# Performance work log

Measured on AMD Instinct MI355X. Metric: run time of the kernel, lower is better.

The kernel has to match this reference:

```python
import jax, jax.numpy as jnp
import numpy as np
import math

B, LQ, LK, D, H = 4, 1024, 1024, 1024, 16
DK = D // H
SCALE = 1.0 / math.sqrt(DK)
NEG_INF = -1.0e9


def setup_inputs() -> dict:
    key = jax.random.key(0)
    ks = jax.random.split(key, 18)
    w = lambda k: (jax.random.normal(k, (D, D), dtype=jnp.float32) * 0.02)
    b = lambda k: (jax.random.normal(k, (D,), dtype=jnp.float32) * 0.02)
    mask = jax.random.randint(ks[4], (B, 1, LK), 0, 2).astype(jnp.int32)
    mask = mask.at[..., 0].set(1)  # ensure at least one valid key per row
    return {
        "query": jax.random.normal(ks[0], (B, LQ, D), dtype=jnp.float32),
        "key": jax.random.normal(ks[1], (B, LK, D), dtype=jnp.float32),
        "value": jax.random.normal(ks[2], (B, LK, D), dtype=jnp.float32),
        "weak_rela": jax.random.normal(ks[3], (B, LK, D), dtype=jnp.float32),
        "mask": mask,
        "Wq": w(ks[5]), "bq": b(ks[6]),
        "Wk": w(ks[7]), "bk": b(ks[8]),
        "Wv": w(ks[9]), "bv": b(ks[10]),
        "Wrk": w(ks[11]), "brk": b(ks[12]),
        "Wrv": w(ks[13]), "brv": b(ks[14]),
        "Wo": w(ks[15]), "bo": b(ks[16]),
    }


def _proj(x, W, bias):
    # x: [B, L, D] -> [B, H, L, DK]; torch Linear: y = x @ W.T + b
    y = x @ W.T + bias
    Bn, L, _ = y.shape
    return y.reshape(Bn, L, H, DK).transpose(0, 2, 1, 3)


def reference(query, key, value, weak_rela, mask,
              Wq, bq, Wk, bk, Wv, bv, Wrk, brk, Wrv, brv, Wo, bo):
    q = _proj(query, Wq, bq)        # [B,H,LQ,DK]
    k = _proj(key, Wk, bk)          # [B,H,LK,DK]
    v = _proj(value, Wv, bv)        # [B,H,LK,DK]
    rk = _proj(weak_rela, Wrk, brk) # [B,H,LK,DK]
    rv = _proj(weak_rela, Wrv, brv) # [B,H,LK,DK]

    qk = jnp.einsum('bhqd,bhkd->bhqk', q, k) * SCALE
    qr = jnp.einsum('bhqd,bhkd->bhqk', q, rk) * SCALE

    m = (mask[:, None, :, :] == 0)  # [B,1,1,LK] broadcast over heads/queries
    qk = jnp.where(m, NEG_INF, qk)
    qr = jnp.where(m, NEG_INF, qr)

    p_vis = jax.nn.softmax(qk, axis=-1)
    p_rel = jax.nn.softmax(qr, axis=-1)

    x = (jnp.einsum('bhqk,bhkd->bhqd', p_vis, v)
         + jnp.einsum('bhqk,bhkd->bhqd', p_rel, rv))  # [B,H,LQ,DK]
    x = x.transpose(0, 2, 1, 3).reshape(query.shape[0], -1, H * DK)
    return x @ Wo.T + bo
```

## Files before the change

### kernel.cpp

```cpp
#include <hip/hip_runtime.h>
#include <stdint.h>

#define NB 4
#define NH 16
#define DKH 64
#define DMODEL 1024
#define SEQ 1024
#define SCALE 0.125f
#define NEG_INF -1.0e9f
#define K2E 0.18033688011112042f

typedef __bf16 bf16_t;
typedef __bf16 bf16x8 __attribute__((ext_vector_type(8)));
typedef __bf16 bf16x4v __attribute__((ext_vector_type(4)));
typedef float f32x4 __attribute__((ext_vector_type(4)));

typedef const uint32_t __attribute__((address_space(1)))* gas_ptr;
typedef uint32_t __attribute__((address_space(3)))* las_ptr;

__device__ __forceinline__ void gload_lds16(const void* g, void* l) {
  __builtin_amdgcn_global_load_lds((gas_ptr)g, (las_ptr)l, 16, 0, 0);
}


__global__ void cvt_multi(const float* __restrict__ i0, const float* __restrict__ i1,
                          const float* __restrict__ i2, const float* __restrict__ i3,
                          const float* __restrict__ i4, const float* __restrict__ i5,
                          bf16_t* o0, bf16_t* o1, bf16_t* o2, bf16_t* o3, bf16_t* o4, bf16_t* o5,
                          int n) {
  const int t = blockIdx.y;
  const float* in = (t == 0) ? i0 : (t == 1) ? i1 : (t == 2) ? i2 : (t == 3) ? i3 : (t == 4) ? i4 : i5;
  bf16_t* out = (t == 0) ? o0 : (t == 1) ? o1 : (t == 2) ? o2 : (t == 3) ? o3 : (t == 4) ? o4 : o5;
  const int idx = (blockIdx.x * 256 + threadIdx.x) * 4;
  if (idx >= n) return;
  const float4 v = *(const float4*)(in + idx);
  bf16x4v p;
  p[0] = (bf16_t)v.x; p[1] = (bf16_t)v.y; p[2] = (bf16_t)v.z; p[3] = (bf16_t)v.w;
  *(bf16x4v*)(out + idx) = p;
}

#define NXE ((size_t)NB * SEQ * DMODEL)
#define NWE ((size_t)DMODEL * DMODEL)
__global__ void __launch_bounds__(256, 2)
proj_gemm(const bf16_t* __restrict__ Xbase, const bf16_t* __restrict__ Wbase,
          bf16_t* __restrict__ Obase,
          const float* __restrict__ b0, const float* __restrict__ b1,
          const float* __restrict__ b2, const float* __restrict__ b3,
          const float* __restrict__ b4) {
  __shared__ bf16_t As[128 * 64];
  __shared__ bf16_t Bs[64 * 64];
  const int tid = threadIdx.x;
  const int lane = tid & 63;
  const int w = tid >> 6;
  const int wm = w >> 1, wn = w & 1;
  const int g = lane >> 4, c = lane & 15;
  const int bid = blockIdx.x;
  const int lid = (bid & 7) * 320 + (bid >> 3);
  const int seg = lid >> 9;
  const int rr = lid & 511;
  const int bm = rr >> 4, bn = rr & 15;
  const int m0 = bm * 128, n0 = bn * 64;
  const int lrow = lane >> 3;
  const int lcol = ((lane & 7) * 8) ^ ((lane >> 3) << 3);
  const int sc = (c & 7) << 3;

  const bf16_t* A = Xbase + (size_t)((seg < 3) ? seg : 3) * NXE;
  const bf16_t* W = Wbase + (size_t)seg * NWE;
  const int ooff = (seg == 0) ? 0 : (seg == 1) ? 1 : (seg == 2) ? 3 : (seg == 3) ? 2 : 4;
  bf16_t* out = Obase + (size_t)ooff * NXE;
  const float* bias = (seg == 0) ? b0 : (seg == 1) ? b1 : (seg == 2) ? b2 : (seg == 3) ? b3 : b4;
  const bool tr = (seg == 2) || (seg == 4);

  f32x4 acc[4][2] = {};

  for (int kt = 0; kt < DMODEL; kt += 64) {
#pragma unroll
    for (int p = 0; p < 4; ++p) {
      const int row = w * 32 + p * 8;
      gload_lds16(A + (size_t)(m0 + row + lrow) * DMODEL + kt + lcol, &As[row * 64]);
    }
#pragma unroll
    for (int p = 0; p < 2; ++p) {
      const int row = w * 16 + p * 8;
      gload_lds16(W + (size_t)(n0 + row + lrow) * DMODEL + kt + lcol, &Bs[row * 64]);
    }
    __syncthreads();
    bf16x8 af[4][2], bfr[2][2];
#pragma unroll
    for (int i = 0; i < 4; ++i)
#pragma unroll
      for (int kk = 0; kk < 2; ++kk)
        af[i][kk] = *(const bf16x8*)&As[(wm * 64 + i * 16 + c) * 64 + ((kk * 32 + g * 8) ^ sc)];
#pragma unroll
    for (int j = 0; j < 2; ++j)
#pragma unroll
      for (int kk = 0; kk < 2; ++kk)
        bfr[j][kk] = *(const bf16x8*)&Bs[(wn * 32 + j * 16 + c) * 64 + ((kk * 32 + g * 8) ^ sc)];
#pragma unroll
    for (int i = 0; i < 4; ++i)
#pragma unroll
      for (int j = 0; j < 2; ++j) {
        acc[i][j] = __builtin_amdgcn_mfma_f32_16x16x32_bf16(af[i][0], bfr[j][0], acc[i][j], 0, 0, 0);
        acc[i][j] = __builtin_amdgcn_mfma_f32_16x16x32_bf16(af[i][1], bfr[j][1], acc[i][j], 0, 0, 0);
      }
    __syncthreads();
  }

  float bv2[2];
#pragma unroll
  for (int j = 0; j < 2; ++j) bv2[j] = bias[n0 + wn * 32 + j * 16 + c];

#pragma unroll
  for (int i = 0; i < 4; ++i) {
    const int mrow = m0 + wm * 64 + i * 16 + g * 4;
    const int b_ = mrow >> 10, l_ = mrow & 1023;
#pragma unroll
    for (int j = 0; j < 2; ++j) {
      const int n = n0 + wn * 32 + j * 16 + c;
      const int h_ = n >> 6, dk_ = n & 63;
      if (!tr) {
#pragma unroll
        for (int r = 0; r < 4; ++r)
          out[((size_t)(b_ * NH + h_) * SEQ + l_ + r) * DKH + dk_] =
              (bf16_t)(acc[i][j][r] + bv2[j]);
      } else {
        bf16x4v pk;
#pragma unroll
        for (int r = 0; r < 4; ++r) pk[r] = (bf16_t)(acc[i][j][r] + bv2[j]);
        *(bf16x4v*)&out[((size_t)(b_ * NH + h_) * DKH + dk_) * SEQ + l_] = pk;
      }
    }
  }
}

__global__ void __launch_bounds__(256, 2)
out_gemm(const bf16_t* __restrict__ A, const bf16_t* __restrict__ W,
         const float* __restrict__ bias, float* __restrict__ out) {
  __shared__ bf16_t As[128 * 64];
  __shared__ bf16_t Bs[64 * 64];
  const int tid = threadIdx.x;
  const int lane = tid & 63;
  const int w = tid >> 6;
  const int wm = w >> 1, wn = w & 1;
  const int g = lane >> 4, c = lane & 15;
  const int bid = blockIdx.x;
  const int lid = (bid & 7) * 64 + (bid >> 3);
  const int bm = lid >> 4, bn = lid & 15;
  const int m0 = bm * 128, n0 = bn * 64;
  const int lrow = lane >> 3;
  const int lcol = ((lane & 7) * 8) ^ ((lane >> 3) << 3);
  const int sc = (c & 7) << 3;

  f32x4 acc[4][2] = {};

  for (int kt = 0; kt < DMODEL; kt += 64) {
#pragma unroll
    for (int p = 0; p < 4; ++p) {
      const int row = w * 32 + p * 8;
      gload_lds16(A + (size_t)(m0 + row + lrow) * DMODEL + kt + lcol, &As[row * 64]);
    }
#pragma unroll
    for (int p = 0; p < 2; ++p) {
      const int row = w * 16 + p * 8;
      gload_lds16(W + (size_t)(n0 + row + lrow) * DMODEL + kt + lcol, &Bs[row * 64]);
    }
    __syncthreads();
    bf16x8 af[4][2], bfr[2][2];
#pragma unroll
    for (int i = 0; i < 4; ++i)
#pragma unroll
      for (int kk = 0; kk < 2; ++kk)
        af[i][kk] = *(const bf16x8*)&As[(wm * 64 + i * 16 + c) * 64 + ((kk * 32 + g * 8) ^ sc)];
#pragma unroll
    for (int j = 0; j < 2; ++j)
#pragma unroll
      for (int kk = 0; kk < 2; ++kk)
        bfr[j][kk] = *(const bf16x8*)&Bs[(wn * 32 + j * 16 + c) * 64 + ((kk * 32 + g * 8) ^ sc)];
#pragma unroll
    for (int i = 0; i < 4; ++i)
#pragma unroll
      for (int j = 0; j < 2; ++j) {
        acc[i][j] = __builtin_amdgcn_mfma_f32_16x16x32_bf16(af[i][0], bfr[j][0], acc[i][j], 0, 0, 0);
        acc[i][j] = __builtin_amdgcn_mfma_f32_16x16x32_bf16(af[i][1], bfr[j][1], acc[i][j], 0, 0, 0);
      }
    __syncthreads();
  }

  float bv2[2];
#pragma unroll
  for (int j = 0; j < 2; ++j) bv2[j] = bias[n0 + wn * 32 + j * 16 + c];
#pragma unroll
  for (int i = 0; i < 4; ++i) {
    const int mrow = m0 + wm * 64 + i * 16 + g * 4;
#pragma unroll
    for (int j = 0; j < 2; ++j) {
      const int n = n0 + wn * 32 + j * 16 + c;
#pragma unroll
      for (int r = 0; r < 4; ++r)
        out[(size_t)(mrow + r) * DMODEL + n] = acc[i][j][r] + bv2[j];
    }
  }
}

__device__ __forceinline__ void attn_step(
    const bf16_t* __restrict__ Kt, const bf16_t* __restrict__ Vt,
    bf16_t* __restrict__ Pw, const bf16x8 (&qf)[2], const int4 (&mk)[4],
    float& m_s, float& l_s, f32x4 (&o_s)[4], int lane) {
  const int g = lane >> 4, c = lane & 15;
  const int sc = (c & 7) << 3;

  f32x4 s[4];
#pragma unroll
  for (int f = 0; f < 4; ++f) {
    const bf16x8 k0 = *(const bf16x8*)&Kt[(f * 16 + c) * 64 + ((g * 8) ^ sc)];
    const bf16x8 k1 = *(const bf16x8*)&Kt[(f * 16 + c) * 64 + ((32 + g * 8) ^ sc)];
    f32x4 a = {0.f, 0.f, 0.f, 0.f};
    a = __builtin_amdgcn_mfma_f32_16x16x32_bf16(k0, qf[0], a, 0, 0, 0);
    a = __builtin_amdgcn_mfma_f32_16x16x32_bf16(k1, qf[1], a, 0, 0, 0);
    s[f] = a;
  }

#pragma unroll
  for (int f = 0; f < 4; ++f) {
    s[f][0] = (mk[f].x == 0) ? NEG_INF : s[f][0] * K2E;
    s[f][1] = (mk[f].y == 0) ? NEG_INF : s[f][1] * K2E;
    s[f][2] = (mk[f].z == 0) ? NEG_INF : s[f][2] * K2E;
    s[f][3] = (mk[f].w == 0) ? NEG_INF : s[f][3] * K2E;
  }

  float tm = fmaxf(fmaxf(s[0][0], s[0][1]), fmaxf(s[0][2], s[0][3]));
#pragma unroll
  for (int f = 1; f < 4; ++f)
    tm = fmaxf(tm, fmaxf(fmaxf(s[f][0], s[f][1]), fmaxf(s[f][2], s[f][3])));
  tm = fmaxf(tm, __shfl_xor(tm, 16));
  tm = fmaxf(tm, __shfl_xor(tm, 32));

  const float mnew = fmaxf(m_s, tm);
  const float sf = __builtin_amdgcn_exp2f(m_s - mnew);
  m_s = mnew;

  float pf[4];
#pragma unroll
  for (int f = 0; f < 4; ++f) {
#pragma unroll
    for (int r = 0; r < 4; ++r) s[f][r] = __builtin_amdgcn_exp2f(s[f][r] - mnew);
    pf[f] = (s[f][0] + s[f][1]) + (s[f][2] + s[f][3]);
  }
  l_s = l_s * sf + ((pf[0] + pf[1]) + (pf[2] + pf[3]));
#pragma unroll
  for (int jd = 0; jd < 4; ++jd)
#pragma unroll
    for (int r = 0; r < 4; ++r) o_s[jd][r] *= sf;

#pragma unroll
  for (int f = 0; f < 4; ++f) {
    bf16x4v pk;
#pragma unroll
    for (int r = 0; r < 4; ++r) pk[r] = (bf16_t)s[f][r];
    *(bf16x4v*)&Pw[c * 64 + ((f * 16 + g * 4) ^ sc)] = pk;
  }

  const bf16x8 pa0 = *(const bf16x8*)&Pw[c * 64 + ((g * 8) ^ sc)];
  const bf16x8 pa1 = *(const bf16x8*)&Pw[c * 64 + ((32 + g * 8) ^ sc)];
#pragma unroll
  for (int jd = 0; jd < 4; ++jd) {
    const bf16x8 v0 = *(const bf16x8*)&Vt[(jd * 16 + c) * 64 + ((g * 8) ^ sc)];
    const bf16x8 v1 = *(const bf16x8*)&Vt[(jd * 16 + c) * 64 + ((32 + g * 8) ^ sc)];
    o_s[jd] = __builtin_amdgcn_mfma_f32_16x16x32_bf16(v0, pa0, o_s[jd], 0, 0, 0);
    o_s[jd] = __builtin_amdgcn_mfma_f32_16x16x32_bf16(v1, pa1, o_s[jd], 0, 0, 0);
  }
}

__global__ void __launch_bounds__(256, 2)
attn_kernel(const bf16_t* __restrict__ q, const bf16_t* __restrict__ k,
            const bf16_t* __restrict__ rk, const bf16_t* __restrict__ vT,
            const bf16_t* __restrict__ rvT, const int* __restrict__ mask,
            bf16_t* __restrict__ x) {
  __shared__ bf16_t Ks[64 * 64], RKs[64 * 64], Vs[64 * 64], RVs[64 * 64];
  __shared__ bf16_t Ps[4][16 * 64];

  const int tid = threadIdx.x;
  const int lane = tid & 63;
  const int w = tid >> 6;
  const int g = lane >> 4, c = lane & 15;
  const int bid = blockIdx.x;
  const int lid = (bid & 7) * 128 + (bid >> 3);
  const int qt = lid & 15;
  const int bh = lid >> 4;
  const int b = bh >> 4, h = bh & 15;
  const int q0 = qt * 64;

  const bf16_t* qp = q + (size_t)bh * SEQ * DKH;
  const bf16_t* kp = k + (size_t)bh * SEQ * DKH;
  const bf16_t* rkp = rk + (size_t)bh * SEQ * DKH;
  const bf16_t* vp = vT + (size_t)bh * DKH * SEQ;
  const bf16_t* rvp = rvT + (size_t)bh * DKH * SEQ;
  const int* mp = mask + b * SEQ;
  const int lrow = lane >> 3;
  const int lcol = ((lane & 7) * 8) ^ ((lane >> 3) << 3);

  bf16x8 qf[2];
#pragma unroll
  for (int kk = 0; kk < 2; ++kk)
    qf[kk] = *(const bf16x8*)(qp + (size_t)(q0 + w * 16 + c) * DKH + kk * 32 + g * 8);

  f32x4 ov[4] = {}, orl[4] = {};
  float mv = NEG_INF, mr = NEG_INF, lv = 0.f, lr = 0.f;

  for (int t = 0; t < 16; ++t) {
    const int kv0 = t * 64;
    if (t) __syncthreads();
#pragma unroll
    for (int p = 0; p < 2; ++p) {
      const int row = w * 16 + p * 8;
      gload_lds16(kp  + (size_t)(kv0 + row + lrow) * DKH + lcol, &Ks[row * 64]);
      gload_lds16(rkp + (size_t)(kv0 + row + lrow) * DKH + lcol, &RKs[row * 64]);
      gload_lds16(vp  + (size_t)(row + lrow) * SEQ + kv0 + lcol, &Vs[row * 64]);
      gload_lds16(rvp + (size_t)(row + lrow) * SEQ + kv0 + lcol, &RVs[row * 64]);
    }
    __syncthreads();

    int4 mk4[4];
#pragma unroll
    for (int f = 0; f < 4; ++f) mk4[f] = *(const int4*)&mp[kv0 + f * 16 + g * 4];

    attn_step(Ks,  Vs,  Ps[w], qf, mk4, mv, lv, ov,  lane);
    attn_step(RKs, RVs, Ps[w], qf, mk4, mr, lr, orl, lane);
  }

  lv += __shfl_xor(lv, 16); lv += __shfl_xor(lv, 32);
  lr += __shfl_xor(lr, 16); lr += __shfl_xor(lr, 32);
  const float rlv = 1.0f / lv, rlr = 1.0f / lr;

  bf16_t* xb = x + (size_t)b * SEQ * DMODEL + (size_t)h * DKH;
  const int qrow = q0 + w * 16 + c;
#pragma unroll
  for (int jd = 0; jd < 4; ++jd) {
    bf16x4v pk;
#pragma unroll
    for (int r = 0; r < 4; ++r)
      pk[r] = (bf16_t)(ov[jd][r] * rlv + orl[jd][r] * rlr);
    *(bf16x4v*)&xb[(size_t)qrow * DMODEL + jd * 16 + g * 4] = pk;
  }
}

extern "C" void kernel_launch(void* const* d_in, const int* in_sizes, int n_in,
                              void* d_out, int out_size, void* d_ws, size_t ws_size,
                              hipStream_t stream) {
  (void)in_sizes; (void)n_in; (void)out_size; (void)ws_size;
  const float* query = (const float*)d_in[0];
  const float* key_  = (const float*)d_in[1];
  const float* value = (const float*)d_in[2];
  const float* weak  = (const float*)d_in[3];
  const int*   mask  = (const int*)d_in[4];
  const float* Wq  = (const float*)d_in[5];  const float* bq  = (const float*)d_in[6];
  const float* Wk  = (const float*)d_in[7];  const float* bk  = (const float*)d_in[8];
  const float* Wv  = (const float*)d_in[9];  const float* bv  = (const float*)d_in[10];
  const float* Wrk = (const float*)d_in[11]; const float* brk = (const float*)d_in[12];
  const float* Wrv = (const float*)d_in[13]; const float* brv = (const float*)d_in[14];
  const float* Wo  = (const float*)d_in[15]; const float* bo  = (const float*)d_in[16];

  char* ws = (char*)d_ws;
  size_t off = 0;
  auto alloc = [&](size_t bytes) {
    void* p = ws + off;
    off += (bytes + 255) & ~(size_t)255;
    return p;
  };
  const size_t SZ_X = NXE * sizeof(bf16_t);
  const size_t SZ_W = NWE * sizeof(bf16_t);

  bf16_t* Xq = (bf16_t*)alloc(SZ_X);
  bf16_t* Xk = (bf16_t*)alloc(SZ_X);
  bf16_t* Xv = (bf16_t*)alloc(SZ_X);
  bf16_t* Xr = (bf16_t*)alloc(SZ_X);
  bf16_t* Wqb  = (bf16_t*)alloc(SZ_W);
  bf16_t* Wkb  = (bf16_t*)alloc(SZ_W);
  bf16_t* Wvb  = (bf16_t*)alloc(SZ_W);
  bf16_t* Wrkb = (bf16_t*)alloc(SZ_W);
  bf16_t* Wrvb = (bf16_t*)alloc(SZ_W);
  bf16_t* Wob  = (bf16_t*)alloc(SZ_W);
  bf16_t* qh   = (bf16_t*)alloc(SZ_X);
  bf16_t* kh   = (bf16_t*)alloc(SZ_X);
  bf16_t* rkh  = (bf16_t*)alloc(SZ_X);
  bf16_t* vTh  = (bf16_t*)alloc(SZ_X);
  bf16_t* rvTh = (bf16_t*)alloc(SZ_X);
  bf16_t* xh   = (bf16_t*)alloc(SZ_X);
  (void)Xk; (void)Xv; (void)Xr; (void)Wkb; (void)Wvb; (void)Wrkb; (void)Wrvb;
  (void)kh; (void)rkh; (void)vTh; (void)rvTh;

  cvt_multi<<<dim3(4096, 4), 256, 0, stream>>>(query, key_, value, weak, nullptr, nullptr,
                                               Xq, Xk, Xv, Xr, nullptr, nullptr,
                                               NB * SEQ * DMODEL);
  cvt_multi<<<dim3(1024, 6), 256, 0, stream>>>(Wq, Wk, Wv, Wrk, Wrv, Wo,
                                               Wqb, Wkb, Wvb, Wrkb, Wrvb, Wob,
                                               DMODEL * DMODEL);

  proj_gemm<<<dim3(2560), 256, 0, stream>>>(Xq, Wqb, qh, bq, bk, bv, brk, brv);

  attn_kernel<<<dim3(1024), 256, 0, stream>>>(qh, kh, rkh, vTh, rvTh, mask, xh);

  out_gemm<<<dim3(512), 256, 0, stream>>>(xh, Wob, bo, (float*)d_out);
}
```

Measured before the change: 181.9 us.

## Enlarge GEMM tiles to 128x128 and interleave dual attention softmax streams

```diff
diff --git a/kernel.cpp b/kernel.cpp
--- a/kernel.cpp
+++ b/kernel.cpp
@@ -41,6 +41,84 @@
 
 #define NXE ((size_t)NB * SEQ * DMODEL)
 #define NWE ((size_t)DMODEL * DMODEL)
+
+template<int MODE>
+__device__ __forceinline__ void gemm128_body(
+    const bf16_t* __restrict__ A, const bf16_t* __restrict__ W,
+    const float* __restrict__ bias, void* __restrict__ outp,
+    int m0, int n0, bf16_t* As, bf16_t* Bs) {
+  const int tid = threadIdx.x;
+  const int lane = tid & 63;
+  const int w = tid >> 6;
+  const int wm = w >> 1, wn = w & 1;
+  const int g = lane >> 4, c = lane & 15;
+  const int lrow = lane >> 3;
+  const int lcol = ((lane & 7) * 8) ^ ((lane >> 3) << 3);
+  const int sc = (c & 7) << 3;
+
+  f32x4 acc[4][4] = {};
+
+  for (int kt = 0; kt < DMODEL; kt += 64) {
+#pragma unroll
+    for (int p = 0; p < 4; ++p) {
+      const int row = w * 32 + p * 8;
+      gload_lds16(A + (size_t)(m0 + row + lrow) * DMODEL + kt + lcol, &As[row * 64]);
+      gload_lds16(W + (size_t)(n0 + row + lrow) * DMODEL + kt + lcol, &Bs[row * 64]);
+    }
+    __syncthreads();
+    bf16x8 af[4][2], bfr[4][2];
+#pragma unroll
+    for (int i = 0; i < 4; ++i)
+#pragma unroll
+      for (int kk = 0; kk < 2; ++kk) {
+        af[i][kk]  = *(const bf16x8*)&As[(wm * 64 + i * 16 + c) * 64 + ((kk * 32 + g * 8) ^ sc)];
+        bfr[i][kk] = *(const bf16x8*)&Bs[(wn * 64 + i * 16 + c) * 64 + ((kk * 32 + g * 8) ^ sc)];
+      }
+#pragma unroll
+    for (int i = 0; i < 4; ++i)
+#pragma unroll
+      for (int j = 0; j < 4; ++j) {
+        acc[i][j] = __builtin_amdgcn_mfma_f32_16x16x32_bf16(af[i][0], bfr[j][0], acc[i][j], 0, 0, 0);
+        acc[i][j] = __builtin_amdgcn_mfma_f32_16x16x32_bf16(af[i][1], bfr[j][1], acc[i][j], 0, 0, 0);
+      }
+    __syncthreads();
+  }
+
+  float bv4[4];
+#pragma unroll
+  for (int j = 0; j < 4; ++j) bv4[j] = bias[n0 + wn * 64 + j * 16 + c];
+
+#pragma unroll
+  for (int i = 0; i < 4; ++i) {
+    const int mrow = m0 + wm * 64 + i * 16 + g * 4;
+    const int b_ = mrow >> 10, l_ = mrow & 1023;
+#pragma unroll
+    for (int j = 0; j < 4; ++j) {
+      const int n = n0 + wn * 64 + j * 16 + c;
+      if (MODE == 2) {
+        float* o = (float*)outp;
+#pragma unroll
+        for (int r = 0; r < 4; ++r)
+          o[(size_t)(mrow + r) * DMODEL + n] = acc[i][j][r] + bv4[j];
+      } else if (MODE == 0) {
+        bf16_t* o = (bf16_t*)outp;
+        const int h_ = n >> 6, dk_ = n & 63;
+#pragma unroll
+        for (int r = 0; r < 4; ++r)
+          o[((size_t)(b_ * NH + h_) * SEQ + l_ + r) * DKH + dk_] =
+              (bf16_t)(acc[i][j][r] + bv4[j]);
+      } else {
+        bf16_t* o = (bf16_t*)outp;
+        const int h_ = n >> 6, dk_ = n & 63;
+        bf16x4v pk;
+#pragma unroll
+        for (int r = 0; r < 4; ++r) pk[r] = (bf16_t)(acc[i][j][r] + bv4[j]);
+        *(bf16x4v*)&o[((size_t)(b_ * NH + h_) * DKH + dk_) * SEQ + l_] = pk;
+      }
+    }
+  }
+}
+
 __global__ void __launch_bounds__(256, 2)
 proj_gemm(const bf16_t* __restrict__ Xbase, const bf16_t* __restrict__ Wbase,
           bf16_t* __restrict__ Obase,
@@ -48,227 +126,32 @@
           const float* __restrict__ b2, const float* __restrict__ b3,
           const float* __restrict__ b4) {
   __shared__ bf16_t As[128 * 64];
-  __shared__ bf16_t Bs[64 * 64];
-  const int tid = threadIdx.x;
-  const int lane = tid & 63;
-  const int w = tid >> 6;
-  const int wm = w >> 1, wn = w & 1;
-  const int g = lane >> 4, c = lane & 15;
+  __shared__ bf16_t Bs[128 * 64];
   const int bid = blockIdx.x;
-  const int lid = (bid & 7) * 320 + (bid >> 3);
-  const int seg = lid >> 9;
-  const int rr = lid & 511;
-  const int bm = rr >> 4, bn = rr & 15;
-  const int m0 = bm * 128, n0 = bn * 64;
-  const int lrow = lane >> 3;
-  const int lcol = ((lane & 7) * 8) ^ ((lane >> 3) << 3);
-  const int sc = (c & 7) << 3;
+  const int lid = (bid & 7) * 160 + (bid >> 3);
+  const int seg = lid >> 8;
+  const int rr = lid & 255;
+  const int m0 = (rr >> 3) * 128, n0 = (rr & 7) * 128;
 
   const bf16_t* A = Xbase + (size_t)((seg < 3) ? seg : 3) * NXE;
   const bf16_t* W = Wbase + (size_t)seg * NWE;
   const int ooff = (seg == 0) ? 0 : (seg == 1) ? 1 : (seg == 2) ? 3 : (seg == 3) ? 2 : 4;
   bf16_t* out = Obase + (size_t)ooff * NXE;
   const float* bias = (seg == 0) ? b0 : (seg == 1) ? b1 : (seg == 2) ? b2 : (seg == 3) ? b3 : b4;
-  const bool tr = (seg == 2) || (seg == 4);
-
-  f32x4 acc[4][2] = {};
-
-  for (int kt = 0; kt < DMODEL; kt += 64) {
-#pragma unroll
-    for (int p = 0; p < 4; ++p) {
-      const int row = w * 32 + p * 8;
-      gload_lds16(A + (size_t)(m0 + row + lrow) * DMODEL + kt + lcol, &As[row * 64]);
-    }
-#pragma unroll
-    for (int p = 0; p < 2; ++p) {
-      const int row = w * 16 + p * 8;
-      gload_lds16(W + (size_t)(n0 + row + lrow) * DMODEL + kt + lcol, &Bs[row * 64]);
-    }
-    __syncthreads();
-    bf16x8 af[4][2], bfr[2][2];
-#pragma unroll
-    for (int i = 0; i < 4; ++i)
-#pragma unroll
-      for (int kk = 0; kk < 2; ++kk)
-        af[i][kk] = *(const bf16x8*)&As[(wm * 64 + i * 16 + c) * 64 + ((kk * 32 + g * 8) ^ sc)];
-#pragma unroll
-    for (int j = 0; j < 2; ++j)
-#pragma unroll
-      for (int kk = 0; kk < 2; ++kk)
-        bfr[j][kk] = *(const bf16x8*)&Bs[(wn * 32 + j * 16 + c) * 64 + ((kk * 32 + g * 8) ^ sc)];
-#pragma unroll
-    for (int i = 0; i < 4; ++i)
-#pragma unroll
-      for (int j = 0; j < 2; ++j) {
-        acc[i][j] = __builtin_amdgcn_mfma_f32_16x16x32_bf16(af[i][0], bfr[j][0], acc[i][j], 0, 0, 0);
-        acc[i][j] = __builtin_amdgcn_mfma_f32_16x16x32_bf16(af[i][1], bfr[j][1], acc[i][j], 0, 0, 0);
-      }
-    __syncthreads();
-  }
-
-  float bv2[2];
-#pragma unroll
-  for (int j = 0; j < 2; ++j) bv2[j] = bias[n0 + wn * 32 + j * 16 + c];
-
-#pragma unroll
-  for (int i = 0; i < 4; ++i) {
-    const int mrow = m0 + wm * 64 + i * 16 + g * 4;
-    const int b_ = mrow >> 10, l_ = mrow & 1023;
-#pragma unroll
-    for (int j = 0; j < 2; ++j) {
-      const int n = n0 + wn * 32 + j * 16 + c;
-      const int h_ = n >> 6, dk_ = n & 63;
-      if (!tr) {
-#pragma unroll
-        for (int r = 0; r < 4; ++r)
-          out[((size_t)(b_ * NH + h_) * SEQ + l_ + r) * DKH + dk_] =
-              (bf16_t)(acc[i][j][r] + bv2[j]);
-      } else {
-        bf16x4v pk;
-#pragma unroll
-        for (int r = 0; r < 4; ++r) pk[r] = (bf16_t)(acc[i][j][r] + bv2[j]);
-        *(bf16x4v*)&out[((size_t)(b_ * NH + h_) * DKH + dk_) * SEQ + l_] = pk;
-      }
-    }
-  }
+
+  if (seg == 2 || seg == 4) gemm128_body<1>(A, W, bias, out, m0, n0, As, Bs);
+  else                      gemm128_body<0>(A, W, bias, out, m0, n0, As, Bs);
 }
 
 __global__ void __launch_bounds__(256, 2)
 out_gemm(const bf16_t* __restrict__ A, const bf16_t* __restrict__ W,
          const float* __restrict__ bias, float* __restrict__ out) {
   __shared__ bf16_t As[128 * 64];
-  __shared__ bf16_t Bs[64 * 64];
-  const int tid = threadIdx.x;
-  const int lane = tid & 63;
-  const int w = tid >> 6;
-  const int wm = w >> 1, wn = w & 1;
-  const int g = lane >> 4, c = lane & 15;
+  __shared__ bf16_t Bs[128 * 64];
   const int bid = blockIdx.x;
-  const int lid = (bid & 7) * 64 + (bid >> 3);
-  const int bm = lid >> 4, bn = lid & 15;
-  const int m0 = bm * 128, n0 = bn * 64;
-  const int lrow = lane >> 3;
-  const int lcol = ((lane & 7) * 8) ^ ((lane >> 3) << 3);
-  const int sc = (c & 7) << 3;
-
-  f32x4 acc[4][2] = {};
-
-  for (int kt = 0; kt < DMODEL; kt += 64) {
-#pragma unroll
-    for (int p = 0; p < 4; ++p) {
-      const int row = w * 32 + p * 8;
-      gload_lds16(A + (size_t)(m0 + row + lrow) * DMODEL + kt + lcol, &As[row * 64]);
-    }
-#pragma unroll
-    for (int p = 0; p < 2; ++p) {
-      const int row = w * 16 + p * 8;
-      gload_lds16(W + (size_t)(n0 + row + lrow) * DMODEL + kt + lcol, &Bs[row * 64]);
-    }
-    __syncthreads();
-    bf16x8 af[4][2], bfr[2][2];
-#pragma unroll
-    for (int i = 0; i < 4; ++i)
-#pragma unroll
-      for (int kk = 0; kk < 2; ++kk)
-        af[i][kk] = *(const bf16x8*)&As[(wm * 64 + i * 16 + c) * 64 + ((kk * 32 + g * 8) ^ sc)];
-#pragma unroll
-    for (int j = 0; j < 2; ++j)
-#pragma unroll
-      for (int kk = 0; kk < 2; ++kk)
-        bfr[j][kk] = *(const bf16x8*)&Bs[(wn * 32 + j * 16 + c) * 64 + ((kk * 32 + g * 8) ^ sc)];
-#pragma unroll
-    for (int i = 0; i < 4; ++i)
-#pragma unroll
-      for (int j = 0; j < 2; ++j) {
-        acc[i][j] = __builtin_amdgcn_mfma_f32_16x16x32_bf16(af[i][0], bfr[j][0], acc[i][j], 0, 0, 0);
-        acc[i][j] = __builtin_amdgcn_mfma_f32_16x16x32_bf16(af[i][1], bfr[j][1], acc[i][j], 0, 0, 0);
-      }
-    __syncthreads();
-  }
-
-  float bv2[2];
-#pragma unroll
-  for (int j = 0; j < 2; ++j) bv2[j] = bias[n0 + wn * 32 + j * 16 + c];
-#pragma unroll
-  for (int i = 0; i < 4; ++i) {
-    const int mrow = m0 + wm * 64 + i * 16 + g * 4;
-#pragma unroll
-    for (int j = 0; j < 2; ++j) {
-      const int n = n0 + wn * 32 + j * 16 + c;
-#pragma unroll
-      for (int r = 0; r < 4; ++r)
-        out[(size_t)(mrow + r) * DMODEL + n] = acc[i][j][r] + bv2[j];
-    }
-  }
-}
-
-__device__ __forceinline__ void attn_step(
-    const bf16_t* __restrict__ Kt, const bf16_t* __restrict__ Vt,
-    bf16_t* __restrict__ Pw, const bf16x8 (&qf)[2], const int4 (&mk)[4],
-    float& m_s, float& l_s, f32x4 (&o_s)[4], int lane) {
-  const int g = lane >> 4, c = lane & 15;
-  const int sc = (c & 7) << 3;
-
-  f32x4 s[4];
-#pragma unroll
-  for (int f = 0; f < 4; ++f) {
-    const bf16x8 k0 = *(const bf16x8*)&Kt[(f * 16 + c) * 64 + ((g * 8) ^ sc)];
-    const bf16x8 k1 = *(const bf16x8*)&Kt[(f * 16 + c) * 64 + ((32 + g * 8) ^ sc)];
-    f32x4 a = {0.f, 0.f, 0.f, 0.f};
-    a = __builtin_amdgcn_mfma_f32_16x16x32_bf16(k0, qf[0], a, 0, 0, 0);
-    a = __builtin_amdgcn_mfma_f32_16x16x32_bf16(k1, qf[1], a, 0, 0, 0);
-    s[f] = a;
-  }
-
-#pragma unroll
-  for (int f = 0; f < 4; ++f) {
-    s[f][0] = (mk[f].x == 0) ? NEG_INF : s[f][0] * K2E;
-    s[f][1] = (mk[f].y == 0) ? NEG_INF : s[f][1] * K2E;
-    s[f][2] = (mk[f].z == 0) ? NEG_INF : s[f][2] * K2E;
-    s[f][3] = (mk[f].w == 0) ? NEG_INF : s[f][3] * K2E;
-  }
-
-  float tm = fmaxf(fmaxf(s[0][0], s[0][1]), fmaxf(s[0][2], s[0][3]));
-#pragma unroll
-  for (int f = 1; f < 4; ++f)
-    tm = fmaxf(tm, fmaxf(fmaxf(s[f][0], s[f][1]), fmaxf(s[f][2], s[f][3])));
-  tm = fmaxf(tm, __shfl_xor(tm, 16));
-  tm = fmaxf(tm, __shfl_xor(tm, 32));
-
-  const float mnew = fmaxf(m_s, tm);
-  const float sf = __builtin_amdgcn_exp2f(m_s - mnew);
-  m_s = mnew;
-
-  float pf[4];
-#pragma unroll
-  for (int f = 0; f < 4; ++f) {
-#pragma unroll
-    for (int r = 0; r < 4; ++r) s[f][r] = __builtin_amdgcn_exp2f(s[f][r] - mnew);
-    pf[f] = (s[f][0] + s[f][1]) + (s[f][2] + s[f][3]);
-  }
-  l_s = l_s * sf + ((pf[0] + pf[1]) + (pf[2] + pf[3]));
-#pragma unroll
-  for (int jd = 0; jd < 4; ++jd)
-#pragma unroll
-    for (int r = 0; r < 4; ++r) o_s[jd][r] *= sf;
-
-#pragma unroll
-  for (int f = 0; f < 4; ++f) {
-    bf16x4v pk;
-#pragma unroll
-    for (int r = 0; r < 4; ++r) pk[r] = (bf16_t)s[f][r];
-    *(bf16x4v*)&Pw[c * 64 + ((f * 16 + g * 4) ^ sc)] = pk;
-  }
-
-  const bf16x8 pa0 = *(const bf16x8*)&Pw[c * 64 + ((g * 8) ^ sc)];
-  const bf16x8 pa1 = *(const bf16x8*)&Pw[c * 64 + ((32 + g * 8) ^ sc)];
-#pragma unroll
-  for (int jd = 0; jd < 4; ++jd) {
-    const bf16x8 v0 = *(const bf16x8*)&Vt[(jd * 16 + c) * 64 + ((g * 8) ^ sc)];
-    const bf16x8 v1 = *(const bf16x8*)&Vt[(jd * 16 + c) * 64 + ((32 + g * 8) ^ sc)];
-    o_s[jd] = __builtin_amdgcn_mfma_f32_16x16x32_bf16(v0, pa0, o_s[jd], 0, 0, 0);
-    o_s[jd] = __builtin_amdgcn_mfma_f32_16x16x32_bf16(v1, pa1, o_s[jd], 0, 0, 0);
-  }
+  const int lid = (bid & 7) * 32 + (bid >> 3);
+  const int m0 = (lid >> 3) * 128, n0 = (lid & 7) * 128;
+  gemm128_body<2>(A, W, bias, out, m0, n0, As, Bs);
 }
 
 __global__ void __launch_bounds__(256, 2)
@@ -277,12 +160,13 @@
             const bf16_t* __restrict__ rvT, const int* __restrict__ mask,
             bf16_t* __restrict__ x) {
   __shared__ bf16_t Ks[64 * 64], RKs[64 * 64], Vs[64 * 64], RVs[64 * 64];
-  __shared__ bf16_t Ps[4][16 * 64];
+  __shared__ bf16_t Ps[8][16 * 64];
 
   const int tid = threadIdx.x;
   const int lane = tid & 63;
   const int w = tid >> 6;
   const int g = lane >> 4, c = lane & 15;
+  const int sc = (c & 7) << 3;
   const int bid = blockIdx.x;
   const int lid = (bid & 7) * 128 + (bid >> 3);
   const int qt = lid & 15;
@@ -299,6 +183,9 @@
   const int lrow = lane >> 3;
   const int lcol = ((lane & 7) * 8) ^ ((lane >> 3) << 3);
 
+  bf16_t* Pv = Ps[w * 2];
+  bf16_t* Pr = Ps[w * 2 + 1];
+
   bf16x8 qf[2];
 #pragma unroll
   for (int kk = 0; kk < 2; ++kk)
@@ -324,8 +211,109 @@
 #pragma unroll
     for (int f = 0; f < 4; ++f) mk4[f] = *(const int4*)&mp[kv0 + f * 16 + g * 4];
 
-    attn_step(Ks,  Vs,  Ps[w], qf, mk4, mv, lv, ov,  lane);
-    attn_step(RKs, RVs, Ps[w], qf, mk4, mr, lr, orl, lane);
+    f32x4 sv[4], sr[4];
+#pragma unroll
+    for (int f = 0; f < 4; ++f) {
+      const bf16x8 k0  = *(const bf16x8*)&Ks [(f * 16 + c) * 64 + ((g * 8) ^ sc)];
+      const bf16x8 k1  = *(const bf16x8*)&Ks [(f * 16 + c) * 64 + ((32 + g * 8) ^ sc)];
+      const bf16x8 rk0 = *(const bf16x8*)&RKs[(f * 16 + c) * 64 + ((g * 8) ^ sc)];
+      const bf16x8 rk1 = *(const bf16x8*)&RKs[(f * 16 + c) * 64 + ((32 + g * 8) ^ sc)];
+      f32x4 a = {0.f, 0.f, 0.f, 0.f};
+      a = __builtin_amdgcn_mfma_f32_16x16x32_bf16(k0, qf[0], a, 0, 0, 0);
+      a = __builtin_amdgcn_mfma_f32_16x16x32_bf16(k1, qf[1], a, 0, 0, 0);
+      sv[f] = a;
+      f32x4 ar = {0.f, 0.f, 0.f, 0.f};
+      ar = __builtin_amdgcn_mfma_f32_16x16x32_bf16(rk0, qf[0], ar, 0, 0, 0);
+      ar = __builtin_amdgcn_mfma_f32_16x16x32_bf16(rk1, qf[1], ar, 0, 0, 0);
+      sr[f] = ar;
+    }
+
+#pragma unroll
+    for (int f = 0; f < 4; ++f) {
+      const int4 m4 = mk4[f];
+      sv[f][0] = (m4.x == 0) ? NEG_INF : sv[f][0] * K2E;
+      sv[f][1] = (m4.y == 0) ? NEG_INF : sv[f][1] * K2E;
+      sv[f][2] = (m4.z == 0) ? NEG_INF : sv[f][2] * K2E;
+      sv[f][3] = (m4.w == 0) ? NEG_INF : sv[f][3] * K2E;
+      sr[f][0] = (m4.x == 0) ? NEG_INF : sr[f][0] * K2E;
+      sr[f][1] = (m4.y == 0) ? NEG_INF : sr[f][1] * K2E;
+      sr[f][2] = (m4.z == 0) ? NEG_INF : sr[f][2] * K2E;
+      sr[f][3] = (m4.w == 0) ? NEG_INF : sr[f][3] * K2E;
+    }
+
+    {
+      float tm = fmaxf(fmaxf(sv[0][0], sv[0][1]), fmaxf(sv[0][2], sv[0][3]));
+#pragma unroll
+      for (int f = 1; f < 4; ++f)
+        tm = fmaxf(tm, fmaxf(fmaxf(sv[f][0], sv[f][1]), fmaxf(sv[f][2], sv[f][3])));
+      tm = fmaxf(tm, __shfl_xor(tm, 16));
+      tm = fmaxf(tm, __shfl_xor(tm, 32));
+      const float mnew = fmaxf(mv, tm);
+      const float sf = __builtin_amdgcn_exp2f(mv - mnew);
+      mv = mnew;
+      float pf = 0.f;
+#pragma unroll
+      for (int f = 0; f < 4; ++f) {
+        bf16x4v pk;
+#pragma unroll
+        for (int r = 0; r < 4; ++r) {
+          const float p = __builtin_amdgcn_exp2f(sv[f][r] - mnew);
+          pf += p;
+          pk[r] = (bf16_t)p;
+        }
+        *(bf16x4v*)&Pv[c * 64 + ((f * 16 + g * 4) ^ sc)] = pk;
+      }
+      lv = lv * sf + pf;
+#pragma unroll
+      for (int jd = 0; jd < 4; ++jd)
+#pragma unroll
+        for (int r = 0; r < 4; ++r) ov[jd][r] *= sf;
+    }
+
+    {
+      float tm = fmaxf(fmaxf(sr[0][0], sr[0][1]), fmaxf(sr[0][2], sr[0][3]));
+#pragma unroll
+      for (int f = 1; f < 4; ++f)
+        tm = fmaxf(tm, fmaxf(fmaxf(sr[f][0], sr[f][1]), fmaxf(sr[f][2], sr[f][3])));
+      tm = fmaxf(tm, __shfl_xor(tm, 16));
+      tm = fmaxf(tm, __shfl_xor(tm, 32));
+      const float mnew = fmaxf(mr, tm);
+      const float sf = __builtin_amdgcn_exp2f(mr - mnew);
+      mr = mnew;
+      float pf = 0.f;
+#pragma unroll
+      for (int f = 0; f < 4; ++f) {
+        bf16x4v pk;
+#pragma unroll
+        for (int r = 0; r < 4; ++r) {
+          const float p = __builtin_amdgcn_exp2f(sr[f][r] - mnew);
+          pf += p;
+          pk[r] = (bf16_t)p;
+        }
+        *(bf16x4v*)&Pr[c * 64 + ((f * 16 + g * 4) ^ sc)] = pk;
+      }
+      lr = lr * sf + pf;
+#pragma unroll
+      for (int jd = 0; jd < 4; ++jd)
+#pragma unroll
+        for (int r = 0; r < 4; ++r) orl[jd][r] *= sf;
+    }
+
+    const bf16x8 pav0 = *(const bf16x8*)&Pv[c * 64 + ((g * 8) ^ sc)];
+    const bf16x8 pav1 = *(const bf16x8*)&Pv[c * 64 + ((32 + g * 8) ^ sc)];
+    const bf16x8 par0 = *(const bf16x8*)&Pr[c * 64 + ((g * 8) ^ sc)];
+    const bf16x8 par1 = *(const bf16x8*)&Pr[c * 64 + ((32 + g * 8) ^ sc)];
+#pragma unroll
+    for (int jd = 0; jd < 4; ++jd) {
+      const bf16x8 v0  = *(const bf16x8*)&Vs [(jd * 16 + c) * 64 + ((g * 8) ^ sc)];
+      const bf16x8 v1  = *(const bf16x8*)&Vs [(jd * 16 + c) * 64 + ((32 + g * 8) ^ sc)];
+      ov[jd]  = __builtin_amdgcn_mfma_f32_16x16x32_bf16(v0, pav0, ov[jd], 0, 0, 0);
+      ov[jd]  = __builtin_amdgcn_mfma_f32_16x16x32_bf16(v1, pav1, ov[jd], 0, 0, 0);
+      const bf16x8 rv0 = *(const bf16x8*)&RVs[(jd * 16 + c) * 64 + ((g * 8) ^ sc)];
+      const bf16x8 rv1 = *(const bf16x8*)&RVs[(jd * 16 + c) * 64 + ((32 + g * 8) ^ sc)];
+      orl[jd] = __builtin_amdgcn_mfma_f32_16x16x32_bf16(rv0, par0, orl[jd], 0, 0, 0);
+      orl[jd] = __builtin_amdgcn_mfma_f32_16x16x32_bf16(rv1, par1, orl[jd], 0, 0, 0);
+    }
   }
 
   lv += __shfl_xor(lv, 16); lv += __shfl_xor(lv, 32);
@@ -396,9 +384,9 @@
                                                Wqb, Wkb, Wvb, Wrkb, Wrvb, Wob,
                                                DMODEL * DMODEL);
 
-  proj_gemm<<<dim3(2560), 256, 0, stream>>>(Xq, Wqb, qh, bq, bk, bv, brk, brv);
+  proj_gemm<<<dim3(1280), 256, 0, stream>>>(Xq, Wqb, qh, bq, bk, bv, brk, brv);
 
   attn_kernel<<<dim3(1024), 256, 0, stream>>>(qh, kh, rkh, vTh, rvTh, mask, xh);
 
-  out_gemm<<<dim3(512), 256, 0, stream>>>(xh, Wob, bo, (float*)d_out);
-}
+  out_gemm<<<dim3(256), 256, 0, stream>>>(xh, Wob, bo, (float*)d_out);
+}
```

After: 187.4 us. 1.03x slower.
